# Kernel tuning notes

Measured on AMD Instinct MI355X. Metric: run time of the kernel, lower is better.

## Reference

```python
import jax, jax.numpy as jnp
import numpy as np

D_MODEL = 1024
D_FF = 4 * D_MODEL
NUM_EXPERTS = 8
TOP_K = 2
B, L = 4, 2048


def setup_inputs() -> dict:
    key = jax.random.key(0)
    ks = jax.random.split(key, 7)
    s = 0.02
    return {
        "x": jax.random.normal(ks[0], (B, L, D_MODEL), dtype=jnp.float32),
        "Wr": jax.random.normal(ks[1], (D_MODEL, NUM_EXPERTS), dtype=jnp.float32) * s,
        "br": jnp.zeros((NUM_EXPERTS,), dtype=jnp.float32),
        "W1": jax.random.normal(ks[2], (NUM_EXPERTS, D_MODEL, D_FF), dtype=jnp.float32) * s,
        "b1": jnp.zeros((NUM_EXPERTS, D_FF), dtype=jnp.float32),
        "W2": jax.random.normal(ks[3], (NUM_EXPERTS, D_FF, D_MODEL), dtype=jnp.float32) * s,
        "b2": jnp.zeros((NUM_EXPERTS, D_MODEL), dtype=jnp.float32),
    }


def reference(x, Wr, br, W1, b1, W2, b2):
    Bb, Ll, D = x.shape
    x_flat = x.reshape(-1, D)                      # [T, D]
    T = x_flat.shape[0]

    # Router: softmax over experts, then top-k and renormalize (matches torch)
    logits = x_flat @ Wr + br                      # [T, E]
    probs = jax.nn.softmax(logits, axis=-1)
    topk_w, topk_idx = jax.lax.top_k(probs, TOP_K)  # [T, K]
    topk_w = topk_w / jnp.sum(topk_w, axis=-1, keepdims=True)

    # Per-token per-expert combine weights: w_full[t, e] = sum_k topk_w[t,k] * (topk_idx[t,k]==e)
    # (top_k indices are distinct, so scatter-add equals the masked-overwrite loop)
    w_full = jnp.zeros((T, NUM_EXPERTS), dtype=x.dtype)
    rows = jnp.arange(T)[:, None]
    w_full = w_full.at[rows, topk_idx].add(topk_w)

    # Dense all-expert MLP (same math as masked per-expert dispatch; dropout is eval/no-op)
    h = jax.nn.gelu(jnp.einsum("td,edf->etf", x_flat, W1) + b1[:, None, :], approximate=False)
    y = jnp.einsum("etf,efd->etd", h, W2) + b2[:, None, :]   # [E, T, D]
    out = jnp.einsum("te,etd->td", w_full, y)                # [T, D]
    return out.reshape(Bb, Ll, D)
```

## Files before the change

kernel.cpp:

```cpp
#include <hip/hip_runtime.h>
#include <hip/hip_bf16.h>

#define T_TOKENS 8192
#define DM 1024
#define DF 4096
#define NE 8
#define NROWS 16384

typedef __attribute__((ext_vector_type(8))) short bf16x8;
typedef __attribute__((ext_vector_type(4))) float f32x4;

__device__ inline unsigned short f2bf(float f) {
  unsigned int u = __builtin_bit_cast(unsigned int, f);
  u = (u + 0x7fffu + ((u >> 16) & 1u)) >> 16;
  return (unsigned short)u;
}

__device__ __forceinline__ void gload16(const unsigned short* g, unsigned short* l) {
  __builtin_amdgcn_global_load_lds(
      (const __attribute__((address_space(1))) unsigned int*)g,
      (__attribute__((address_space(3))) unsigned int*)l,
      16, 0, 0);
}

__global__ void router_kernel(const float* __restrict__ x,
                              const float* __restrict__ Wr,
                              const float* __restrict__ br,
                              int* __restrict__ ctrl,
                              int* __restrict__ tope,
                              float* __restrict__ topw) {
  const int wid = threadIdx.x >> 6;
  const int lane = threadIdx.x & 63;
  const int t = blockIdx.x * 4 + wid;
  const float* xr = x + (size_t)t * DM;
  float a[NE];
#pragma unroll
  for (int e = 0; e < NE; ++e) a[e] = 0.f;
#pragma unroll
  for (int it = 0; it < 4; ++it) {
    const int d0 = it * 256 + lane * 4;
    const float4 xv = *(const float4*)(xr + d0);
    const float xs[4] = {xv.x, xv.y, xv.z, xv.w};
#pragma unroll
    for (int j = 0; j < 4; ++j) {
      const float4 wa = *(const float4*)(Wr + (size_t)(d0 + j) * NE);
      const float4 wb = *(const float4*)(Wr + (size_t)(d0 + j) * NE + 4);
      a[0] += xs[j] * wa.x; a[1] += xs[j] * wa.y;
      a[2] += xs[j] * wa.z; a[3] += xs[j] * wa.w;
      a[4] += xs[j] * wb.x; a[5] += xs[j] * wb.y;
      a[6] += xs[j] * wb.z; a[7] += xs[j] * wb.w;
    }
  }
#pragma unroll
  for (int off = 32; off > 0; off >>= 1) {
#pragma unroll
    for (int e = 0; e < NE; ++e) a[e] += __shfl_xor(a[e], off);
  }
  if (lane == 0) {
    float lg[NE];
    float m = -1e30f;
#pragma unroll
    for (int e = 0; e < NE; ++e) { lg[e] = a[e] + br[e]; m = fmaxf(m, lg[e]); }
    float p[NE];
#pragma unroll
    for (int e = 0; e < NE; ++e) p[e] = expf(lg[e] - m);
    int i0 = 0;
#pragma unroll
    for (int e = 1; e < NE; ++e) if (p[e] > p[i0]) i0 = e;
    int i1 = (i0 == 0) ? 1 : 0;
#pragma unroll
    for (int e = 0; e < NE; ++e) if (e != i0 && p[e] > p[i1]) i1 = e;
    const float s = p[i0] + p[i1];
    tope[2 * t] = i0;
    tope[2 * t + 1] = i1;
    topw[2 * t] = p[i0] / s;
    topw[2 * t + 1] = p[i1] / s;
    atomicAdd(&ctrl[i0], 1);
    atomicAdd(&ctrl[i1], 1);
  }
}

__global__ void scan_kernel(int* __restrict__ ctrl) {
  if (threadIdx.x == 0 && blockIdx.x == 0) {
    int off = 0;
    for (int e = 0; e < NE; ++e) {
      ctrl[8 + e] = off;
      ctrl[20 + e] = off;
      off += ctrl[e];
    }
    ctrl[16] = off;
  }
}

__global__ void place_kernel(const int* __restrict__ tope,
                             const float* __restrict__ topw,
                             int* __restrict__ ctrl,
                             int* __restrict__ rowlist,
                             float* __restrict__ roww) {
  const int t = blockIdx.x * blockDim.x + threadIdx.x;
#pragma unroll
  for (int k = 0; k < 2; ++k) {
    const int e = tope[2 * t + k];
    const int pos = atomicAdd(&ctrl[20 + e], 1);
    rowlist[pos] = t;
    roww[pos] = topw[2 * t + k];
  }
}

__global__ void cvt_x_kernel(const float* __restrict__ x,
                             unsigned short* __restrict__ xb) {
  const size_t i = ((size_t)blockIdx.x * blockDim.x + threadIdx.x) * 4;
  const float4 v = *(const float4*)(x + i);
  ushort4 o;
  o.x = f2bf(v.x); o.y = f2bf(v.y); o.z = f2bf(v.z); o.w = f2bf(v.w);
  *(ushort4*)(xb + i) = o;
}

__global__ void transpose_cvt_kernel(const float* __restrict__ in,
                                     unsigned short* __restrict__ outp,
                                     int R, int C) {
  __shared__ float tile[64][65];
  const int e = blockIdx.z;
  const int r0 = blockIdx.y * 64;
  const int c0 = blockIdx.x * 64;
  const float* src = in + ((size_t)e * R + r0) * C + c0;
#pragma unroll
  for (int i = 0; i < 16; ++i) {
    const int rr = (threadIdx.x >> 6) + i * 4;
    const int cc = threadIdx.x & 63;
    tile[rr][cc] = src[(size_t)rr * C + cc];
  }
  __syncthreads();
  unsigned short* dst = outp + ((size_t)e * C + c0) * R + r0;
#pragma unroll
  for (int i = 0; i < 8; ++i) {
    const int rr = (threadIdx.x >> 5) + i * 8;
    const int cc = (threadIdx.x & 31) * 2;
    const unsigned int lo = f2bf(tile[cc][rr]);
    const unsigned int hi = f2bf(tile[cc + 1][rr]);
    *(unsigned int*)(dst + (size_t)rr * R + cc) = lo | (hi << 16);
  }
}

__global__ __launch_bounds__(256, 2) void gemm1_kernel(
    const unsigned short* __restrict__ xb,
    const unsigned short* __restrict__ w1t,
    const float* __restrict__ b1,
    const int* __restrict__ ctrl,
    const int* __restrict__ rowlist,
    unsigned short* __restrict__ h) {
  const int e = blockIdx.z;
  const int count = ctrl[e];
  const int mt = blockIdx.y;
  if (mt * 128 >= count) return;
  const int off = ctrl[8 + e];
  const int n0 = blockIdx.x * 128;
  const int tid = threadIdx.x;
  const int wid = tid >> 6;
  const int lane = tid & 63;
  const int wm = (wid & 1) * 64;
  const int wn = (wid >> 1) * 64;
  const int q = lane >> 4;
  const int l16 = lane & 15;
  const int rl = lane >> 3;
  const int ch = lane & 7;

  __shared__ __attribute__((aligned(16))) unsigned short lA[128 * 64];
  __shared__ __attribute__((aligned(16))) unsigned short lB[128 * 64];

  const unsigned short* aBase[4];
  const unsigned short* bBase[4];
  unsigned short* lABase[4];
  unsigned short* lBBase[4];
#pragma unroll
  for (int i = 0; i < 4; ++i) {
    const int r = wid * 32 + i * 8 + rl;
    int rr = mt * 128 + r;
    if (rr >= count) rr = count - 1;
    const int tok = rowlist[off + rr];
    aBase[i] = xb + (size_t)tok * DM + ch * 8;
    bBase[i] = w1t + ((size_t)e * DF + n0 + r) * DM + ch * 8;
    lABase[i] = &lA[(wid * 32 + i * 8) * 64];
    lBBase[i] = &lB[(wid * 32 + i * 8) * 64];
  }

  f32x4 acc[4][4];
  const f32x4 z = {0.f, 0.f, 0.f, 0.f};
#pragma unroll
  for (int im = 0; im < 4; ++im)
#pragma unroll
    for (int in = 0; in < 4; ++in) acc[im][in] = z;

  for (int k0 = 0; k0 < DM; k0 += 64) {
#pragma unroll
    for (int i = 0; i < 4; ++i) gload16(aBase[i] + k0, lABase[i]);
#pragma unroll
    for (int i = 0; i < 4; ++i) gload16(bBase[i] + k0, lBBase[i]);
    __syncthreads();
#pragma unroll
    for (int ks = 0; ks < 2; ++ks) {
      bf16x8 af[4], bfr[4];
#pragma unroll
      for (int im = 0; im < 4; ++im)
        af[im] = *(const bf16x8*)&lA[(wm + im * 16 + l16) * 64 + ks * 32 + q * 8];
#pragma unroll
      for (int in = 0; in < 4; ++in)
        bfr[in] = *(const bf16x8*)&lB[(wn + in * 16 + l16) * 64 + ks * 32 + q * 8];
#pragma unroll
      for (int im = 0; im < 4; ++im)
#pragma unroll
        for (int in = 0; in < 4; ++in)
          acc[im][in] = __builtin_amdgcn_mfma_f32_16x16x32_bf16(
              af[im], bfr[in], acc[im][in], 0, 0, 0);
    }
    __syncthreads();
  }

#pragma unroll
  for (int in = 0; in < 4; ++in) {
    const int col = n0 + wn + in * 16 + l16;
    const float bias = b1[(size_t)e * DF + col];
#pragma unroll
    for (int im = 0; im < 4; ++im) {
      const int rbase = mt * 128 + wm + im * 16 + q * 4;
#pragma unroll
      for (int r2 = 0; r2 < 4; ++r2) {
        const int r = rbase + r2;
        if (r < count) {
          const float v = acc[im][in][r2] + bias;
          const float g = 0.5f * v * (1.0f + erff(v * 0.70710678118f));
          h[((size_t)(off + r)) * DF + col] = f2bf(g);
        }
      }
    }
  }
}

__global__ __launch_bounds__(256, 2) void gemm2_kernel(
    const unsigned short* __restrict__ h,
    const unsigned short* __restrict__ w2t,
    const float* __restrict__ b2,
    const int* __restrict__ ctrl,
    const int* __restrict__ rowlist,
    const float* __restrict__ roww,
    float* __restrict__ out) {
  const int e = blockIdx.z;
  const int count = ctrl[e];
  const int mt = blockIdx.y;
  if (mt * 128 >= count) return;
  const int off = ctrl[8 + e];
  const int n0 = blockIdx.x * 128;
  const int tid = threadIdx.x;
  const int wid = tid >> 6;
  const int lane = tid & 63;
  const int wm = (wid & 1) * 64;
  const int wn = (wid >> 1) * 64;
  const int q = lane >> 4;
  const int l16 = lane & 15;
  const int rl = lane >> 3;
  const int ch = lane & 7;

  __shared__ __attribute__((aligned(16))) unsigned short lA[128 * 64];
  __shared__ __attribute__((aligned(16))) unsigned short lB[128 * 64];

  const unsigned short* aBase[4];
  const unsigned short* bBase[4];
  unsigned short* lABase[4];
  unsigned short* lBBase[4];
#pragma unroll
  for (int i = 0; i < 4; ++i) {
    const int r = wid * 32 + i * 8 + rl;
    int rr = mt * 128 + r;
    if (rr >= count) rr = count - 1;
    aBase[i] = h + (size_t)(off + rr) * DF + ch * 8;
    bBase[i] = w2t + ((size_t)e * DM + n0 + r) * DF + ch * 8;
    lABase[i] = &lA[(wid * 32 + i * 8) * 64];
    lBBase[i] = &lB[(wid * 32 + i * 8) * 64];
  }

  f32x4 acc[4][4];
  const f32x4 z = {0.f, 0.f, 0.f, 0.f};
#pragma unroll
  for (int im = 0; im < 4; ++im)
#pragma unroll
    for (int in = 0; in < 4; ++in) acc[im][in] = z;

  for (int k0 = 0; k0 < DF; k0 += 64) {
#pragma unroll
    for (int i = 0; i < 4; ++i) gload16(aBase[i] + k0, lABase[i]);
#pragma unroll
    for (int i = 0; i < 4; ++i) gload16(bBase[i] + k0, lBBase[i]);
    __syncthreads();
#pragma unroll
    for (int ks = 0; ks < 2; ++ks) {
      bf16x8 af[4], bfr[4];
#pragma unroll
      for (int im = 0; im < 4; ++im)
        af[im] = *(const bf16x8*)&lA[(wm + im * 16 + l16) * 64 + ks * 32 + q * 8];
#pragma unroll
      for (int in = 0; in < 4; ++in)
        bfr[in] = *(const bf16x8*)&lB[(wn + in * 16 + l16) * 64 + ks * 32 + q * 8];
#pragma unroll
      for (int im = 0; im < 4; ++im)
#pragma unroll
        for (int in = 0; in < 4; ++in)
          acc[im][in] = __builtin_amdgcn_mfma_f32_16x16x32_bf16(
              af[im], bfr[in], acc[im][in], 0, 0, 0);
    }
    __syncthreads();
  }

#pragma unroll
  for (int in = 0; in < 4; ++in) {
    const int col = n0 + wn + in * 16 + l16;
    const float bias = b2[(size_t)e * DM + col];
#pragma unroll
    for (int im = 0; im < 4; ++im) {
      const int rbase = mt * 128 + wm + im * 16 + q * 4;
#pragma unroll
      for (int r2 = 0; r2 < 4; ++r2) {
        const int r = rbase + r2;
        if (r < count) {
          const int pos = off + r;
          const int tok = rowlist[pos];
          const float w = roww[pos];
          atomicAdd(&out[(size_t)tok * DM + col], (acc[im][in][r2] + bias) * w);
        }
      }
    }
  }
}

extern "C" void kernel_launch(void* const* d_in, const int* in_sizes, int n_in,
                              void* d_out, int out_size, void* d_ws, size_t ws_size,
                              hipStream_t stream) {
  const float* x  = (const float*)d_in[0];
  const float* Wr = (const float*)d_in[1];
  const float* br = (const float*)d_in[2];
  const float* W1 = (const float*)d_in[3];
  const float* b1 = (const float*)d_in[4];
  const float* W2 = (const float*)d_in[5];
  const float* b2 = (const float*)d_in[6];
  float* out = (float*)d_out;

  char* p = (char*)d_ws;
  auto alloc = [&](size_t bytes) -> char* {
    char* r = p;
    p += (bytes + 255) & ~(size_t)255;
    return r;
  };
  int* ctrl = (int*)alloc(1024);
  int* tope = (int*)alloc((size_t)2 * T_TOKENS * 4);
  float* topw = (float*)alloc((size_t)2 * T_TOKENS * 4);
  int* rowlist = (int*)alloc((size_t)NROWS * 4);
  float* roww = (float*)alloc((size_t)NROWS * 4);
  unsigned short* xb  = (unsigned short*)alloc((size_t)T_TOKENS * DM * 2);
  unsigned short* w1t = (unsigned short*)alloc((size_t)NE * DF * DM * 2);
  unsigned short* w2t = (unsigned short*)alloc((size_t)NE * DM * DF * 2);
  unsigned short* h   = (unsigned short*)alloc((size_t)NROWS * DF * 2);
  if ((size_t)(p - (char*)d_ws) > ws_size) return;

  hipMemsetAsync(ctrl, 0, 1024, stream);
  hipMemsetAsync(d_out, 0, sizeof(float) * (size_t)out_size, stream);

  router_kernel<<<T_TOKENS / 4, 256, 0, stream>>>(x, Wr, br, ctrl, tope, topw);
  scan_kernel<<<1, 64, 0, stream>>>(ctrl);
  place_kernel<<<T_TOKENS / 256, 256, 0, stream>>>(tope, topw, ctrl, rowlist, roww);
  cvt_x_kernel<<<(T_TOKENS * DM / 4) / 256, 256, 0, stream>>>(x, xb);
  transpose_cvt_kernel<<<dim3(DF / 64, DM / 64, NE), 256, 0, stream>>>(W1, w1t, DM, DF);
  transpose_cvt_kernel<<<dim3(DM / 64, DF / 64, NE), 256, 0, stream>>>(W2, w2t, DF, DM);
  gemm1_kernel<<<dim3(DF / 128, 64, NE), 256, 0, stream>>>(xb, w1t, b1, ctrl, rowlist, h);
  gemm2_kernel<<<dim3(DM / 128, 64, NE), 256, 0, stream>>>(h, w2t, b2, ctrl, rowlist, roww, out);
}
```

Measured before the change: 1.176 ms.

## Replace atomic scatter-add in gemm2 with bf16 expert outputs and a gather-combine kernel

gemm2 now writes per-row expert outputs as bf16 into a buffer that reuses the W1-transposed workspace. A new combine kernel gathers each token's two rows through a position map and forms the weighted sum, so the fp32 atomics and the output memset are gone. The x-to-bf16 conversion is folded into the router kernel, which removes one launch and one extra read of x. The trade-off is an extra bf16 round trip for the expert outputs, which costs some precision, plus one more kernel launch.

```diff
diff --git a/kernel.cpp b/kernel.cpp
--- a/kernel.cpp
+++ b/kernel.cpp
@@ -16,6 +16,11 @@
   return (unsigned short)u;
 }
 
+__device__ inline float bf2f(unsigned short s) {
+  unsigned int u = ((unsigned int)s) << 16;
+  return __builtin_bit_cast(float, u);
+}
+
 __device__ __forceinline__ void gload16(const unsigned short* g, unsigned short* l) {
   __builtin_amdgcn_global_load_lds(
       (const __attribute__((address_space(1))) unsigned int*)g,
@@ -28,11 +33,13 @@
                               const float* __restrict__ br,
                               int* __restrict__ ctrl,
                               int* __restrict__ tope,
-                              float* __restrict__ topw) {
+                              float* __restrict__ topw,
+                              unsigned short* __restrict__ xb) {
   const int wid = threadIdx.x >> 6;
   const int lane = threadIdx.x & 63;
   const int t = blockIdx.x * 4 + wid;
   const float* xr = x + (size_t)t * DM;
+  unsigned short* xbr = xb + (size_t)t * DM;
   float a[NE];
 #pragma unroll
   for (int e = 0; e < NE; ++e) a[e] = 0.f;
@@ -40,6 +47,9 @@
   for (int it = 0; it < 4; ++it) {
     const int d0 = it * 256 + lane * 4;
     const float4 xv = *(const float4*)(xr + d0);
+    ushort4 o;
+    o.x = f2bf(xv.x); o.y = f2bf(xv.y); o.z = f2bf(xv.z); o.w = f2bf(xv.w);
+    *(ushort4*)(xbr + d0) = o;
     const float xs[4] = {xv.x, xv.y, xv.z, xv.w};
 #pragma unroll
     for (int j = 0; j < 4; ++j) {
@@ -96,7 +106,8 @@
                              const float* __restrict__ topw,
                              int* __restrict__ ctrl,
                              int* __restrict__ rowlist,
-                             float* __restrict__ roww) {
+                             float* __restrict__ roww,
+                             int* __restrict__ posmap) {
   const int t = blockIdx.x * blockDim.x + threadIdx.x;
 #pragma unroll
   for (int k = 0; k < 2; ++k) {
@@ -104,16 +115,8 @@
     const int pos = atomicAdd(&ctrl[20 + e], 1);
     rowlist[pos] = t;
     roww[pos] = topw[2 * t + k];
-  }
-}
-
-__global__ void cvt_x_kernel(const float* __restrict__ x,
-                             unsigned short* __restrict__ xb) {
-  const size_t i = ((size_t)blockIdx.x * blockDim.x + threadIdx.x) * 4;
-  const float4 v = *(const float4*)(x + i);
-  ushort4 o;
-  o.x = f2bf(v.x); o.y = f2bf(v.y); o.z = f2bf(v.z); o.w = f2bf(v.w);
-  *(ushort4*)(xb + i) = o;
+    posmap[2 * t + k] = pos;
+  }
 }
 
 __global__ void transpose_cvt_kernel(const float* __restrict__ in,
@@ -241,9 +244,7 @@
     const unsigned short* __restrict__ w2t,
     const float* __restrict__ b2,
     const int* __restrict__ ctrl,
-    const int* __restrict__ rowlist,
-    const float* __restrict__ roww,
-    float* __restrict__ out) {
+    unsigned short* __restrict__ y) {
   const int e = blockIdx.z;
   const int count = ctrl[e];
   const int mt = blockIdx.y;
@@ -321,14 +322,31 @@
       for (int r2 = 0; r2 < 4; ++r2) {
         const int r = rbase + r2;
         if (r < count) {
-          const int pos = off + r;
-          const int tok = rowlist[pos];
-          const float w = roww[pos];
-          atomicAdd(&out[(size_t)tok * DM + col], (acc[im][in][r2] + bias) * w);
+          y[(size_t)(off + r) * DM + col] = f2bf(acc[im][in][r2] + bias);
         }
       }
     }
   }
+}
+
+__global__ void combine_kernel(const unsigned short* __restrict__ y,
+                               const int* __restrict__ posmap,
+                               const float* __restrict__ topw,
+                               float* __restrict__ out) {
+  const int t = blockIdx.x;
+  const int c = threadIdx.x * 4;
+  const int p0 = posmap[2 * t];
+  const int p1 = posmap[2 * t + 1];
+  const float w0 = topw[2 * t];
+  const float w1 = topw[2 * t + 1];
+  const ushort4 a = *(const ushort4*)(y + (size_t)p0 * DM + c);
+  const ushort4 b = *(const ushort4*)(y + (size_t)p1 * DM + c);
+  float4 o;
+  o.x = w0 * bf2f(a.x) + w1 * bf2f(b.x);
+  o.y = w0 * bf2f(a.y) + w1 * bf2f(b.y);
+  o.z = w0 * bf2f(a.z) + w1 * bf2f(b.z);
+  o.w = w0 * bf2f(a.w) + w1 * bf2f(b.w);
+  *(float4*)(out + (size_t)t * DM + c) = o;
 }
 
 extern "C" void kernel_launch(void* const* d_in, const int* in_sizes, int n_in,
@@ -354,21 +372,23 @@
   float* topw = (float*)alloc((size_t)2 * T_TOKENS * 4);
   int* rowlist = (int*)alloc((size_t)NROWS * 4);
   float* roww = (float*)alloc((size_t)NROWS * 4);
+  int* posmap = (int*)alloc((size_t)NROWS * 4);
   unsigned short* xb  = (unsigned short*)alloc((size_t)T_TOKENS * DM * 2);
   unsigned short* w1t = (unsigned short*)alloc((size_t)NE * DF * DM * 2);
   unsigned short* w2t = (unsigned short*)alloc((size_t)NE * DM * DF * 2);
   unsigned short* h   = (unsigned short*)alloc((size_t)NROWS * DF * 2);
   if ((size_t)(p - (char*)d_ws) > ws_size) return;
 
+  unsigned short* y = w1t;
+
   hipMemsetAsync(ctrl, 0, 1024, stream);
-  hipMemsetAsync(d_out, 0, sizeof(float) * (size_t)out_size, stream);
-
-  router_kernel<<<T_TOKENS / 4, 256, 0, stream>>>(x, Wr, br, ctrl, tope, topw);
+
+  router_kernel<<<T_TOKENS / 4, 256, 0, stream>>>(x, Wr, br, ctrl, tope, topw, xb);
   scan_kernel<<<1, 64, 0, stream>>>(ctrl);
-  place_kernel<<<T_TOKENS / 256, 256, 0, stream>>>(tope, topw, ctrl, rowlist, roww);
-  cvt_x_kernel<<<(T_TOKENS * DM / 4) / 256, 256, 0, stream>>>(x, xb);
+  place_kernel<<<T_TOKENS / 256, 256, 0, stream>>>(tope, topw, ctrl, rowlist, roww, posmap);
   transpose_cvt_kernel<<<dim3(DF / 64, DM / 64, NE), 256, 0, stream>>>(W1, w1t, DM, DF);
   transpose_cvt_kernel<<<dim3(DM / 64, DF / 64, NE), 256, 0, stream>>>(W2, w2t, DF, DM);
   gemm1_kernel<<<dim3(DF / 128, 64, NE), 256, 0, stream>>>(xb, w1t, b1, ctrl, rowlist, h);
-  gemm2_kernel<<<dim3(DM / 128, 64, NE), 256, 0, stream>>>(h, w2t, b2, ctrl, rowlist, roww, out);
-}
+  gemm2_kernel<<<dim3(DM / 128, 64, NE), 256, 0, stream>>>(h, w2t, b2, ctrl, y);
+  combine_kernel<<<T_TOKENS, 256, 0, stream>>>(y, posmap, topw, out);
+}
```

New measurement: 1.123 ms. 1.05x faster.
